# Kernel tuning notes

Measured on AMD Instinct MI355X. Metric: run time of the kernel, lower is better.

## Reference

```python
import jax, jax.numpy as jnp
import numpy as np

N, M, D, G = 8192, 8192, 512, 10

def _embed_distance_matrix(dist):
    # classical MDS embedding: ||e_i - e_j||^2 == dist[i,j]**2
    g = dist.shape[0]
    d2 = dist ** 2
    J = np.eye(g) - np.ones((g, g)) / g
    B = -0.5 * J @ d2 @ J
    w, v = np.linalg.eigh(B)
    w = np.clip(w, 0.0, None)
    return (v * np.sqrt(w)).astype(np.float32)  # [g, g]

def setup_inputs() -> dict:
    key = jax.random.key(0)
    k1, k2, k3, k4 = jax.random.split(key, 4)
    X = jax.random.normal(k1, (N, D), dtype=jnp.float32)
    Z = jax.random.normal(k2, (M, D), dtype=jnp.float32)
    groupsX = jax.random.randint(k3, (N,), 0, G)
    groupsZ = jax.random.randint(k4, (M,), 0, G)
    group_distances = np.ones((G, G)) - np.eye(G)
    embedding = jnp.asarray(_embed_distance_matrix(group_distances))
    return {
        "X": X, "Z": Z,
        "groupsX": groupsX, "groupsZ": groupsZ,
        "embedding": embedding,
        "sigma": jnp.float32(1.0),
        "lengthscale": jnp.float32(1.0),
        "group_diff_param": jnp.float32(1.0),
    }

def _pairwise_sqdist(a, b):
    # ||a_i - b_j||^2 via GEMM; avoids the O(N*M*d) diff tensor
    aa = jnp.sum(a * a, axis=-1)  # [N]
    bb = jnp.sum(b * b, axis=-1)  # [M]
    return aa[:, None] + bb[None, :] - 2.0 * (a @ b.T)  # [N, M]

def reference(X, Z, groupsX, groupsZ, embedding, sigma, lengthscale, group_diff_param):
    p = X.shape[-1]
    ex = embedding[groupsX]  # [N, g]
    ez = embedding[groupsZ]  # [M, g]
    dist = _pairwise_sqdist(X, Z)           # [N, M]
    gdist = _pairwise_sqdist(ex, ez)        # [N, M]
    val = 1.0 / (jnp.abs(group_diff_param) * gdist + 1.0)
    dist_scaled = dist / lengthscale ** 2
    K = sigma ** 2 * jnp.exp(-0.5 * dist_scaled * val) * val ** (0.5 * p)
    return K  # [N, M], matches torch result.transpose(-1, 0)
```

## Files before the change

kernel.cpp:

```cpp
#include <hip/hip_runtime.h>
#include <hip/hip_bf16.h>
#include <cstdint>
#include <cstddef>

#define NROWS 8192
#define MCOLS 8192
#define DDIM  512
#define GRP   10

using f32x4 = __attribute__((ext_vector_type(4))) float;

typedef const __attribute__((address_space(1))) void* gas_ptr;
typedef __attribute__((address_space(3))) void* las_ptr;

__global__ __launch_bounds__(256) void prep_all(const float* __restrict__ X,
                                                const float* __restrict__ Z,
                                                uint16_t* __restrict__ Xa,
                                                uint16_t* __restrict__ Za,
                                                float* __restrict__ xx,
                                                float* __restrict__ zz,
                                                const float* __restrict__ emb,
                                                const float* __restrict__ sigma_p,
                                                const float* __restrict__ ls_p,
                                                const float* __restrict__ gdp_p,
                                                float2* __restrict__ tab) {
    int row = blockIdx.x;
    int t = threadIdx.x;
    if (row == 2 * NROWS) {
        if (t >= GRP * GRP) return;
        int a = t / GRP, b = t % GRP;
        float gd = 0.0f;
        #pragma unroll
        for (int g = 0; g < GRP; ++g) {
            float d = emb[a * GRP + g] - emb[b * GRP + g];
            gd += d * d;
        }
        float val = 1.0f / (fabsf(*gdp_p) * gd + 1.0f);
        float ls = *ls_p;
        float sg = *sigma_p;
        tab[t] = make_float2(-0.5f * val / (ls * ls),
                             sg * sg * powf(val, 0.5f * (float)DDIM));
        return;
    }
    const float* src;
    uint16_t* dst;
    float* sums;
    int r;
    if (row < NROWS) {
        r = row; src = X + (size_t)r * DDIM; dst = Xa + (size_t)r * (DDIM / 2); sums = xx;
    } else {
        r = row - NROWS; src = Z + (size_t)r * DDIM; dst = Za + (size_t)r * (DDIM / 2); sums = zz;
    }
    float2 p = ((const float2*)src)[t];
    int packed = __builtin_amdgcn_cvt_pk_fp8_f32(p.x, p.y, 0, false);
    dst[t] = (uint16_t)packed;
    float s = p.x * p.x + p.y * p.y;
    #pragma unroll
    for (int off = 32; off > 0; off >>= 1) s += __shfl_down(s, off, 64);
    __shared__ float ws[4];
    if ((t & 63) == 0) ws[t >> 6] = s;
    __syncthreads();
    if (t == 0) sums[r] = ws[0] + ws[1] + ws[2] + ws[3];
}

__global__ __launch_bounds__(512, 2) void mggp_gemm(
    const uint8_t* __restrict__ Xa, const uint8_t* __restrict__ Za,
    const float* __restrict__ xx, const float* __restrict__ zz,
    const int* __restrict__ gX, const int* __restrict__ gZ,
    const float2* __restrict__ tab,
    float* __restrict__ out) {

    extern __shared__ __align__(16) uint8_t lds[];

    const int tid  = threadIdx.x;
    const int lane = tid & 63;
    const int w    = tid >> 6;
    const int wr   = w >> 2;
    const int wc   = w & 3;
    const int m    = lane & 15;
    const int q    = lane >> 4;

    const int lin = blockIdx.x;
    const int st  = lin >> 6;
    const int wi  = lin & 63;
    const int bx  = (st & 3) * 8 + (wi & 7);
    const int by  = (st >> 2) * 8 + (wi >> 3);
    const int brow = by * 256;
    const int bcol = bx * 256;

    auto stageA = [&](int skt, int skh) {
        const int slot = ((skt & 1) * 2 + skh) * 16384;
        #pragma unroll
        for (int l = 0; l < 2; ++l) {
            int s = l * 512 + tid;
            int r = s >> 2;
            int pc = (s & 3) ^ ((r >> 1) & 3);
            const uint8_t* src = Xa + (size_t)(brow + r) * DDIM + skt * 128 + skh * 64 + pc * 16;
            __builtin_amdgcn_global_load_lds((gas_ptr)src, (las_ptr)(lds + slot + s * 16), 16, 0, 0);
        }
    };
    auto stageB = [&](int skt, int skh) {
        const int slot = 65536 + ((skt & 1) * 2 + skh) * 16384;
        #pragma unroll
        for (int l = 0; l < 2; ++l) {
            int s = l * 512 + tid;
            int r = s >> 2;
            int pc = (s & 3) ^ ((r >> 1) & 3);
            const uint8_t* src = Za + (size_t)(bcol + r) * DDIM + skt * 128 + skh * 64 + pc * 16;
            __builtin_amdgcn_global_load_lds((gas_ptr)src, (las_ptr)(lds + slot + s * 16), 16, 0, 0);
        }
    };

    f32x4 acc[8][4];
    #pragma unroll
    for (int ti = 0; ti < 8; ++ti)
        #pragma unroll
        for (int tj = 0; tj < 4; ++tj)
            #pragma unroll
            for (int e = 0; e < 4; ++e) acc[ti][tj][e] = 0.0f;

    stageA(0, 0); stageB(0, 0);
    stageA(0, 1); stageB(0, 1);
    stageA(1, 0); stageB(1, 0);
    asm volatile("s_waitcnt vmcnt(8)" ::: "memory");
    __builtin_amdgcn_s_barrier();

    const int f2m = ((m >> 1) & 3) << 1;

    #pragma unroll
    for (int P = 0; P < 16; ++P) {
        const int kt  = P >> 2;
        const int kk  = P & 3;
        const int buf = kt & 1;
        const int kh  = kk >> 1;
        const int kl  = kk & 1;
        const int slotA = (buf * 2 + kh) * 16384;
        const int slotB = 65536 + slotA;
        const int pgl = ((kl * 4 + q) ^ f2m) * 8;

        const uint8_t* abase = lds + slotA + (wr * 128 + m) * 64 + pgl;
        const uint8_t* bbase = lds + slotB + (wc * 64 + m) * 64 + pgl;
        long aF[8], bF[4];
        #pragma unroll
        for (int ti = 0; ti < 8; ++ti) aF[ti] = *(const long*)(abase + ti * 1024);
        #pragma unroll
        for (int tj = 0; tj < 4; ++tj) bF[tj] = *(const long*)(bbase + tj * 1024);

        if (P <= 9) {
            const int h   = 6 + P;
            const int skt = h >> 2;
            const int skh = (h >> 1) & 1;
            if ((h & 1) == 0) stageA(skt, skh); else stageB(skt, skh);
        }

        __builtin_amdgcn_s_barrier();
        asm volatile("s_waitcnt lgkmcnt(0)" ::: "memory");
        __builtin_amdgcn_sched_barrier(0);

        __builtin_amdgcn_s_setprio(1);
        #pragma unroll
        for (int ti = 0; ti < 8; ++ti)
            #pragma unroll
            for (int tj = 0; tj < 4; ++tj)
                acc[ti][tj] = __builtin_amdgcn_mfma_f32_16x16x32_fp8_fp8(
                    aF[ti], bF[tj], acc[ti][tj], 0, 0, 0);
        __builtin_amdgcn_s_setprio(0);

        if (P == 1 || P == 3 || P == 5 || P == 7 || P == 9)
            asm volatile("s_waitcnt vmcnt(8)" ::: "memory");
        else if (P == 11)
            asm volatile("s_waitcnt vmcnt(4)" ::: "memory");
        else if (P == 13)
            asm volatile("s_waitcnt vmcnt(0)" ::: "memory");
        __builtin_amdgcn_s_barrier();
    }

    float zzv[4];
    int   gbv[4];
    #pragma unroll
    for (int tj = 0; tj < 4; ++tj) {
        int j = bcol + wc * 64 + tj * 16 + m;
        zzv[tj] = zz[j];
        gbv[tj] = gZ[j];
    }
    #pragma unroll
    for (int ti = 0; ti < 8; ++ti) {
        #pragma unroll
        for (int rg = 0; rg < 4; ++rg) {
            int i = brow + wr * 128 + ti * 16 + q * 4 + rg;
            float xxi = xx[i];
            int   ga  = gX[i] * GRP;
            float* orow = out + (size_t)i * MCOLS + bcol + wc * 64 + m;
            #pragma unroll
            for (int tj = 0; tj < 4; ++tj) {
                float dot  = acc[ti][tj][rg];
                float dist = xxi + zzv[tj] - 2.0f * dot;
                float2 tc  = tab[ga + gbv[tj]];
                orow[tj * 16] = tc.y * __expf(dist * tc.x);
            }
        }
    }
}

extern "C" void kernel_launch(void* const* d_in, const int* in_sizes, int n_in,
                              void* d_out, int out_size, void* d_ws, size_t ws_size,
                              hipStream_t stream) {
    const float* X     = (const float*)d_in[0];
    const float* Z     = (const float*)d_in[1];
    const int*   gX    = (const int*)d_in[2];
    const int*   gZ    = (const int*)d_in[3];
    const float* emb   = (const float*)d_in[4];
    const float* sigma = (const float*)d_in[5];
    const float* ls    = (const float*)d_in[6];
    const float* gdp   = (const float*)d_in[7];

    char* ws = (char*)d_ws;
    const size_t XA_OFF  = 0;
    const size_t ZA_OFF  = XA_OFF + (size_t)NROWS * DDIM;
    const size_t XX_OFF  = ZA_OFF + (size_t)MCOLS * DDIM;
    const size_t ZZ_OFF  = XX_OFF + (size_t)NROWS * 4;
    const size_t TAB_OFF = ZZ_OFF + (size_t)MCOLS * 4;

    uint8_t* Xa  = (uint8_t*)(ws + XA_OFF);
    uint8_t* Za  = (uint8_t*)(ws + ZA_OFF);
    float* xx    = (float*)(ws + XX_OFF);
    float* zz    = (float*)(ws + ZZ_OFF);
    float2* tab  = (float2*)(ws + TAB_OFF);

    static bool inited = false;
    if (!inited) {
        (void)hipFuncSetAttribute((const void*)mggp_gemm,
                                  hipFuncAttributeMaxDynamicSharedMemorySize, 131072);
        inited = true;
    }

    prep_all<<<2 * NROWS + 1, 256, 0, stream>>>(X, Z, (uint16_t*)Xa, (uint16_t*)Za,
                                                xx, zz, emb, sigma, ls, gdp, tab);
    mggp_gemm<<<1024, 512, 131072, stream>>>(Xa, Za, xx, zz, gX, gZ, tab, (float*)d_out);
}
```

Measured before the change: 367.9 us.

## Pre-permute FP8 K layout, use 128-bit LDS reads and triple-buffered K pipeline

The prep kernel now writes FP8 rows with a permuted byte order within each 64-byte K chunk. This lets each lane fetch two MFMA K-slices with a single 16-byte LDS read instead of two 8-byte reads. The GEMM main loop becomes 8 K-steps of 64 bytes over a 3-slot ring buffer (96 KB LDS instead of 128 KB), issuing two steps ahead, with one barrier per step and no explicit lgkmcnt wait. Block-to-tile mapping is also remapped by XCD to improve L2 locality. The risk is that dropping the lgkmcnt wait relies on the compiler inserting it, and the reduced prefetch depth could expose load latency.

```diff
diff --git a/kernel.cpp b/kernel.cpp
--- a/kernel.cpp
+++ b/kernel.cpp
@@ -9,6 +9,7 @@
 #define GRP   10
 
 using f32x4 = __attribute__((ext_vector_type(4))) float;
+using i64x2 = __attribute__((ext_vector_type(2))) long;
 
 typedef const __attribute__((address_space(1))) void* gas_ptr;
 typedef __attribute__((address_space(3))) void* las_ptr;
@@ -53,7 +54,11 @@
     }
     float2 p = ((const float2*)src)[t];
     int packed = __builtin_amdgcn_cvt_pk_fp8_f32(p.x, p.y, 0, false);
-    dst[t] = (uint16_t)packed;
+    int b    = 2 * t;
+    int g    = (b >> 3) & 7;
+    int P    = ((g & 3) << 1) | (g >> 2);
+    int phys = (b & 0x1C0) | (P << 3) | (b & 7);
+    dst[phys >> 1] = (uint16_t)packed;
     float s = p.x * p.x + p.y * p.y;
     #pragma unroll
     for (int off = 32; off > 0; off >>= 1) s += __shfl_down(s, off, 64);
@@ -81,33 +86,21 @@
     const int q    = lane >> 4;
 
     const int lin = blockIdx.x;
-    const int st  = lin >> 6;
-    const int wi  = lin & 63;
-    const int bx  = (st & 3) * 8 + (wi & 7);
-    const int by  = (st >> 2) * 8 + (wi >> 3);
+    const int xcd = lin & 7;
+    const int i0  = lin >> 3;
+    const int by  = (xcd >> 1) * 8 + (i0 >> 4);
+    const int bx  = (xcd & 1) * 16 + (i0 & 15);
     const int brow = by * 256;
     const int bcol = bx * 256;
 
-    auto stageA = [&](int skt, int skh) {
-        const int slot = ((skt & 1) * 2 + skh) * 16384;
+    auto stage = [&](const uint8_t* __restrict__ base, int rowoff, int kt, int ldsoff) {
         #pragma unroll
         for (int l = 0; l < 2; ++l) {
-            int s = l * 512 + tid;
-            int r = s >> 2;
-            int pc = (s & 3) ^ ((r >> 1) & 3);
-            const uint8_t* src = Xa + (size_t)(brow + r) * DDIM + skt * 128 + skh * 64 + pc * 16;
-            __builtin_amdgcn_global_load_lds((gas_ptr)src, (las_ptr)(lds + slot + s * 16), 16, 0, 0);
-        }
-    };
-    auto stageB = [&](int skt, int skh) {
-        const int slot = 65536 + ((skt & 1) * 2 + skh) * 16384;
-        #pragma unroll
-        for (int l = 0; l < 2; ++l) {
-            int s = l * 512 + tid;
-            int r = s >> 2;
-            int pc = (s & 3) ^ ((r >> 1) & 3);
-            const uint8_t* src = Za + (size_t)(bcol + r) * DDIM + skt * 128 + skh * 64 + pc * 16;
-            __builtin_amdgcn_global_load_lds((gas_ptr)src, (las_ptr)(lds + slot + s * 16), 16, 0, 0);
+            int s  = l * 512 + tid;
+            int r  = s >> 2;
+            int cg = (s & 3) ^ ((r >> 1) & 3);
+            const uint8_t* src = base + (size_t)(rowoff + r) * DDIM + kt * 64 + cg * 16;
+            __builtin_amdgcn_global_load_lds((gas_ptr)src, (las_ptr)(lds + ldsoff + s * 16), 16, 0, 0);
         }
     };
 
@@ -119,60 +112,53 @@
             #pragma unroll
             for (int e = 0; e < 4; ++e) acc[ti][tj][e] = 0.0f;
 
-    stageA(0, 0); stageB(0, 0);
-    stageA(0, 1); stageB(0, 1);
-    stageA(1, 0); stageB(1, 0);
-    asm volatile("s_waitcnt vmcnt(8)" ::: "memory");
+    stage(Xa, brow, 0, 0);
+    stage(Za, bcol, 0, 49152);
+    stage(Xa, brow, 1, 16384);
+    stage(Za, bcol, 1, 49152 + 16384);
+    asm volatile("s_waitcnt vmcnt(4)" ::: "memory");
     __builtin_amdgcn_s_barrier();
 
-    const int f2m = ((m >> 1) & 3) << 1;
-
-    #pragma unroll
-    for (int P = 0; P < 16; ++P) {
-        const int kt  = P >> 2;
-        const int kk  = P & 3;
-        const int buf = kt & 1;
-        const int kh  = kk >> 1;
-        const int kl  = kk & 1;
-        const int slotA = (buf * 2 + kh) * 16384;
-        const int slotB = 65536 + slotA;
-        const int pgl = ((kl * 4 + q) ^ f2m) * 8;
-
-        const uint8_t* abase = lds + slotA + (wr * 128 + m) * 64 + pgl;
-        const uint8_t* bbase = lds + slotB + (wc * 64 + m) * 64 + pgl;
-        long aF[8], bF[4];
-        #pragma unroll
-        for (int ti = 0; ti < 8; ++ti) aF[ti] = *(const long*)(abase + ti * 1024);
-        #pragma unroll
-        for (int tj = 0; tj < 4; ++tj) bF[tj] = *(const long*)(bbase + tj * 1024);
-
-        if (P <= 9) {
-            const int h   = 6 + P;
-            const int skt = h >> 2;
-            const int skh = (h >> 1) & 1;
-            if ((h & 1) == 0) stageA(skt, skh); else stageB(skt, skh);
+    const int swz  = (m >> 1) & 3;
+    const int aoff = (wr * 128 + m) * 64 + ((q ^ swz) * 16);
+    const int boff = (wc * 64 + m) * 64 + ((q ^ swz) * 16);
+
+    #pragma unroll
+    for (int kt = 0; kt < 8; ++kt) {
+        const int bi   = kt % 3;
+        const int abuf = bi * 16384;
+        const int bbuf = 49152 + bi * 16384;
+
+        i64x2 aF[8], bF[4];
+        #pragma unroll
+        for (int ti = 0; ti < 8; ++ti)
+            aF[ti] = *(const i64x2*)(lds + abuf + aoff + ti * 1024);
+        #pragma unroll
+        for (int tj = 0; tj < 4; ++tj)
+            bF[tj] = *(const i64x2*)(lds + bbuf + boff + tj * 1024);
+
+        if (kt <= 5) {
+            const int bn = (kt + 2) % 3;
+            stage(Xa, brow, kt + 2, bn * 16384);
+            stage(Za, bcol, kt + 2, 49152 + bn * 16384);
         }
 
         __builtin_amdgcn_s_barrier();
-        asm volatile("s_waitcnt lgkmcnt(0)" ::: "memory");
-        __builtin_amdgcn_sched_barrier(0);
 
         __builtin_amdgcn_s_setprio(1);
         #pragma unroll
-        for (int ti = 0; ti < 8; ++ti)
+        for (int kk = 0; kk < 2; ++kk)
             #pragma unroll
-            for (int tj = 0; tj < 4; ++tj)
-                acc[ti][tj] = __builtin_amdgcn_mfma_f32_16x16x32_fp8_fp8(
-                    aF[ti], bF[tj], acc[ti][tj], 0, 0, 0);
+            for (int ti = 0; ti < 8; ++ti)
+                #pragma unroll
+                for (int tj = 0; tj < 4; ++tj)
+                    acc[ti][tj] = __builtin_amdgcn_mfma_f32_16x16x32_fp8_fp8(
+                        aF[ti][kk], bF[tj][kk], acc[ti][tj], 0, 0, 0);
         __builtin_amdgcn_s_setprio(0);
 
-        if (P == 1 || P == 3 || P == 5 || P == 7 || P == 9)
-            asm volatile("s_waitcnt vmcnt(8)" ::: "memory");
-        else if (P == 11)
-            asm volatile("s_waitcnt vmcnt(4)" ::: "memory");
-        else if (P == 13)
-            asm volatile("s_waitcnt vmcnt(0)" ::: "memory");
-        __builtin_amdgcn_s_barrier();
+        if (kt <= 5)      asm volatile("s_waitcnt vmcnt(4)" ::: "memory");
+        else if (kt == 6) asm volatile("s_waitcnt vmcnt(0)" ::: "memory");
+        if (kt < 7) __builtin_amdgcn_s_barrier();
     }
 
     float zzv[4];
@@ -230,11 +216,11 @@
     static bool inited = false;
     if (!inited) {
         (void)hipFuncSetAttribute((const void*)mggp_gemm,
-                                  hipFuncAttributeMaxDynamicSharedMemorySize, 131072);
+                                  hipFuncAttributeMaxDynamicSharedMemorySize, 98304);
         inited = true;
     }
 
     prep_all<<<2 * NROWS + 1, 256, 0, stream>>>(X, Z, (uint16_t*)Xa, (uint16_t*)Za,
                                                 xx, zz, emb, sigma, ls, gdp, tab);
-    mggp_gemm<<<1024, 512, 131072, stream>>>(Xa, Za, xx, zz, gX, gZ, tab, (float*)d_out);
+    mggp_gemm<<<1024, 512, 98304, stream>>>(Xa, Za, xx, zz, gX, gZ, tab, (float*)d_out);
 }
```

After: 354.1 us. 1.04x faster.
